# Kernel tuning notes

Hardware: AMD Instinct MI355X
Metric: run time of the kernel (lower is better)

Reference implementation:

```python
import jax, jax.numpy as jnp
import numpy as np

D = 512       # input_embedding_dimensions
H = 2         # num_heads
HD = D // H   # head_dim = 256
B = 16
S = 1194      # max_sequence_length


def setup_inputs() -> dict:
    key = jax.random.key(0)
    k1, k2, k3, k4, k5 = jax.random.split(key, 5)
    scale_in = 1.0 / np.sqrt(D)
    return {
        "positional_embeddings": jax.random.normal(k1, (B, S, D), dtype=jnp.float32),
        "W_qkv": jax.random.uniform(k2, (D, 3 * D), minval=-scale_in, maxval=scale_in, dtype=jnp.float32),
        "b_qkv": jax.random.uniform(k3, (3 * D,), minval=-scale_in, maxval=scale_in, dtype=jnp.float32),
        "W_out": jax.random.uniform(k4, (D, D), minval=-scale_in, maxval=scale_in, dtype=jnp.float32),
        "b_out": jax.random.uniform(k5, (D,), minval=-scale_in, maxval=scale_in, dtype=jnp.float32),
    }


def reference(positional_embeddings, W_qkv, b_qkv, W_out, b_out):
    x = positional_embeddings              # [B, S, D]
    b, s, _ = x.shape
    qkv = x @ W_qkv + b_qkv                # [B, S, 3D]
    q, k, v = jnp.split(qkv, 3, axis=-1)

    def split_heads(t):
        return t.reshape(b, s, H, HD).transpose(0, 2, 1, 3)  # [B, H, S, HD]

    q, k, v = split_heads(q), split_heads(k), split_heads(v)
    scores = jnp.einsum("bhqd,bhkd->bhqk", q, k) / jnp.sqrt(jnp.float32(HD))
    causal = jnp.tril(jnp.ones((s, s), dtype=bool))          # [S, S]
    scores = jnp.where(causal[None, None, :, :], scores, -jnp.inf)
    att = jax.nn.softmax(scores, axis=-1)                    # [B, H, S, S]
    out = jnp.einsum("bhqk,bhkd->bhqd", att, v)              # [B, H, S, HD]
    out = out.transpose(0, 2, 1, 3).reshape(b, s, D)         # [B, S, D]
    return out @ W_out + b_out
```

## Files before the change

kernel.cpp:

```cpp
#include <hip/hip_runtime.h>
#include <stdint.h>

#define D_    512
#define H_    2
#define HD_   256
#define B_    16
#define S_    1194
#define MTOK  19104
#define MPAD  19200
#define SPAD  1216
#define NQKV  1536
#define NKT   38
#define LOG2E 1.44269504088896340736f

typedef unsigned short u16;
typedef __attribute__((ext_vector_type(8))) short bf16x8;
typedef __attribute__((ext_vector_type(4))) float f32x4;

__device__ inline u16 f2bf(float x) {
  union { float f; unsigned u; } c; c.f = x;
  unsigned r = c.u + 0x7fffu + ((c.u >> 16) & 1u);
  return (u16)(r >> 16);
}

__device__ inline void async_copy16(void* lds, const void* g) {
  __builtin_amdgcn_global_load_lds(
      (__attribute__((address_space(1))) void*)(g),
      (__attribute__((address_space(3))) void*)(lds),
      16, 0, 0);
}

__global__ void convert_kernel(const float* __restrict__ X,
                               const float* __restrict__ Wqkv,
                               const float* __restrict__ Wout,
                               u16* __restrict__ Xf,
                               u16* __restrict__ Wqf,
                               u16* __restrict__ Wof) {
  const int NXG = MPAD * 64;
  const int NQG = 12 * 8 * 16 * 64;
  const int NOG = 4 * 8 * 16 * 64;
  const int TOT = NXG + NQG + NOG;
  int stride = gridDim.x * blockDim.x;
  for (int g = blockIdx.x * blockDim.x + threadIdx.x; g < TOT; g += stride) {
    if (g < NXG) {
      int lane = g & 63, f = (g >> 6) & 15, kt = (g >> 10) & 7, mt = g >> 13;
      int i = mt * 128 + (f & 7) * 16 + (lane & 15);
      int k = kt * 64 + (f >> 3) * 32 + (lane >> 4) * 8;
      bf16x8 o;
      if (i < MTOK) {
        f32x4 v0 = *(const f32x4*)&X[(size_t)i * 512 + k];
        f32x4 v1 = *(const f32x4*)&X[(size_t)i * 512 + k + 4];
#pragma unroll
        for (int e = 0; e < 4; ++e) { o[e] = (short)f2bf(v0[e]); o[4 + e] = (short)f2bf(v1[e]); }
      } else {
#pragma unroll
        for (int e = 0; e < 8; ++e) o[e] = 0;
      }
      *(bf16x8*)&Xf[(size_t)g * 8] = o;
    } else if (g < NXG + NQG) {
      int gg = g - NXG;
      int lane = gg & 63, f = (gg >> 6) & 15, kt = (gg >> 10) & 7, nt = gg >> 13;
      int j = nt * 128 + (f & 7) * 16 + (lane & 15);
      int k = kt * 64 + (f >> 3) * 32 + (lane >> 4) * 8;
      bf16x8 o;
#pragma unroll
      for (int e = 0; e < 8; ++e) o[e] = (short)f2bf(Wqkv[(size_t)(k + e) * NQKV + j]);
      *(bf16x8*)&Wqf[(size_t)gg * 8] = o;
    } else {
      int gg = g - NXG - NQG;
      int lane = gg & 63, f = (gg >> 6) & 15, kt = (gg >> 10) & 7, nt = gg >> 13;
      int j = nt * 128 + (f & 7) * 16 + (lane & 15);
      int k = kt * 64 + (f >> 3) * 32 + (lane >> 4) * 8;
      bf16x8 o;
#pragma unroll
      for (int e = 0; e < 8; ++e) o[e] = (short)f2bf(Wout[(size_t)(k + e) * 512 + j]);
      *(bf16x8*)&Wof[(size_t)gg * 8] = o;
    }
  }
}

template<int MODE>
__global__ __launch_bounds__(256, 2) void gemm_kernel(
    const u16* __restrict__ Af, const u16* __restrict__ Bf,
    const float* __restrict__ bias, int nb,
    u16* __restrict__ Qb, u16* __restrict__ Kf, u16* __restrict__ Vf,
    float* __restrict__ Cout)
{
  __shared__ u16 ldsA[16 * 512];
  __shared__ u16 ldsB[16 * 512];

  const int t  = threadIdx.x;
  const int l  = t & 63;
  const int w  = t >> 6;
  const int lr = l >> 4, lc = l & 15;

  const int nwg = gridDim.x;
  const int qq = nwg >> 3, rr8 = nwg & 7;
  const int xcd = blockIdx.x & 7, off = blockIdx.x >> 3;
  const int wgid = (xcd < rr8 ? xcd * (qq + 1) : rr8 * (qq + 1) + (xcd - rr8) * qq) + off;
  const int m0 = (wgid / nb) * 128;
  const int n0 = (wgid % nb) * 128;

  const u16* pA = Af + ((size_t)(m0 >> 7) * 128 + w) * 512 + l * 8;
  const u16* pB = Bf + ((size_t)(n0 >> 7) * 128 + w) * 512 + l * 8;

  f32x4 acc[4][4] = {};

  for (int kt = 0; kt < 8; ++kt) {
    __syncthreads();
    const u16* qA = pA + kt * 8192;
    const u16* qB = pB + kt * 8192;
#pragma unroll
    for (int c = 0; c < 4; ++c) {
      async_copy16(&ldsA[(c * 4 + w) * 512], qA + c * 2048);
      async_copy16(&ldsB[(c * 4 + w) * 512], qB + c * 2048);
    }
    __syncthreads();
#pragma unroll
    for (int kk = 0; kk < 2; ++kk) {
      bf16x8 af[4], bfr[4];
#pragma unroll
      for (int m = 0; m < 4; ++m)
        af[m] = *(bf16x8*)&ldsA[((kk * 8 + (w >> 1) * 4 + m) * 64 + l) * 8];
#pragma unroll
      for (int n = 0; n < 4; ++n)
        bfr[n] = *(bf16x8*)&ldsB[((kk * 8 + (w & 1) * 4 + n) * 64 + l) * 8];
      __builtin_amdgcn_s_setprio(1);
#pragma unroll
      for (int m = 0; m < 4; ++m)
#pragma unroll
        for (int n = 0; n < 4; ++n)
          acc[m][n] = __builtin_amdgcn_mfma_f32_16x16x32_bf16(af[m], bfr[n], acc[m][n], 0, 0, 0);
      __builtin_amdgcn_s_setprio(0);
    }
  }

  int jv[4]; float bj[4];
#pragma unroll
  for (int n = 0; n < 4; ++n) { jv[n] = n0 + (w & 1) * 64 + n * 16 + lc; bj[n] = bias[jv[n]]; }

#pragma unroll
  for (int m = 0; m < 4; ++m) {
#pragma unroll
    for (int r = 0; r < 4; ++r) {
      int i = m0 + (w >> 1) * 64 + m * 16 + lr * 4 + r;
      if (i >= MTOK) continue;
      if (MODE == 0) {
        int b = i / S_, s = i - b * S_;
        int stK  = s >> 5;
        int nfs  = (s >> 4) & 1;
        int lisK = s & 15;
        int lvhi = (s >> 3) & 3;
        int es   = s & 7;
#pragma unroll
        for (int n = 0; n < 4; ++n) {
          int j = jv[n];
          int which = j >> 9, h = (j >> 8) & 1, d = j & 255;
          int bh = b * H_ + h;
          u16 v = f2bf(acc[m][n][r] + bj[n]);
          if (which == 0) {
            Qb[((size_t)(bh * SPAD + s)) * HD_ + d] = v;
          } else if (which == 1) {
            Kf[(((size_t)(bh * NKT + stK)) * 16 + (d >> 5) * 2 + nfs) * 512 +
               (((d >> 3) & 3) * 16 + lisK) * 8 + (d & 7)] = v;
          } else {
            Vf[(((size_t)(bh * NKT + stK)) * 16 + (d >> 4)) * 512 +
               (lvhi * 16 + (d & 15)) * 8 + es] = v;
          }
        }
      } else {
#pragma unroll
        for (int n = 0; n < 4; ++n)
          Cout[(size_t)i * D_ + jv[n]] = acc[m][n][r] + bj[n];
      }
    }
  }
}

__global__ __launch_bounds__(256, 2) void attn_kernel(
    const u16* __restrict__ Qb, const u16* __restrict__ Kf,
    const u16* __restrict__ Vf, u16* __restrict__ Obf)
{
  __shared__ u16 ldsK[2][16 * 512];
  __shared__ u16 ldsP[4][16 * 36];

  const int id   = blockIdx.x;
  const int xcd  = id & 7;
  const int slot = id >> 3;
  const int bh   = xcd + 8 * (slot / 19);
  const int qt   = 18 - (slot % 19);
  const int q0   = qt * 64;
  const int nkv  = 2 * qt + 2;
  const int t  = threadIdx.x, l = t & 63, w = t >> 6;
  const int lr = l >> 4, lc = l & 15;
  const int wq0 = q0 + w * 16;
  const int qrow_l = wq0 + lc;

  bf16x8 qf[8];
  const u16* qbase = Qb + (size_t)(bh * SPAD + qrow_l) * HD_ + lr * 8;
#pragma unroll
  for (int kb = 0; kb < 8; ++kb)
    qf[kb] = *(const bf16x8*)(qbase + kb * 32);

  f32x4 oacc[16] = {};
  float mrow = -1e30f, lsum = 0.f;

  {
    const u16* kb_ = Kf + (((size_t)(bh * NKT)) * 16 + w) * 512 + l * 8;
#pragma unroll
    for (int c = 0; c < 4; ++c)
      async_copy16(&ldsK[0][(c * 4 + w) * 512], kb_ + c * 2048);
  }
  __syncthreads();

  for (int kt = 0; kt < nkv; ++kt) {
    const int cur = kt & 1;

    bf16x8 vfr[16];
    {
      const u16* vb_ = Vf + (((size_t)(bh * NKT + kt)) * 16) * 512 + l * 8;
#pragma unroll
      for (int nf = 0; nf < 16; ++nf)
        vfr[nf] = *(const bf16x8*)(vb_ + nf * 512);
    }

    if (kt + 1 < nkv) {
      const u16* kb_ = Kf + (((size_t)(bh * NKT + kt + 1)) * 16 + w) * 512 + l * 8;
#pragma unroll
      for (int c = 0; c < 4; ++c)
        async_copy16(&ldsK[cur ^ 1][(c * 4 + w) * 512], kb_ + c * 2048);
    }

    f32x4 sacc[2] = {};
    __builtin_amdgcn_s_setprio(1);
#pragma unroll
    for (int kb = 0; kb < 8; ++kb) {
#pragma unroll
      for (int nf = 0; nf < 2; ++nf) {
        bf16x8 kf = *(bf16x8*)&ldsK[cur][((kb * 2 + nf) * 64 + l) * 8];
        sacc[nf] = __builtin_amdgcn_mfma_f32_16x16x32_bf16(kf, qf[kb], sacc[nf], 0, 0, 0);
      }
    }
    __builtin_amdgcn_s_setprio(0);

    const int kv0 = kt * 32;
    float sv[2][4];
    float pm = -1e30f;
    if (kv0 + 31 <= wq0) {
#pragma unroll
      for (int nf = 0; nf < 2; ++nf)
#pragma unroll
        for (int r = 0; r < 4; ++r) {
          float v = sacc[nf][r] * 0.0625f;
          sv[nf][r] = v;
          pm = fmaxf(pm, v);
        }
    } else {
#pragma unroll
      for (int nf = 0; nf < 2; ++nf)
#pragma unroll
        for (int r = 0; r < 4; ++r) {
          int kv = kv0 + nf * 16 + lr * 4 + r;
          float v = ((kv <= qrow_l) && (kv < S_)) ? sacc[nf][r] * 0.0625f : -1e30f;
          sv[nf][r] = v;
          pm = fmaxf(pm, v);
        }
    }
    pm = fmaxf(pm, __shfl_xor(pm, 16));
    pm = fmaxf(pm, __shfl_xor(pm, 32));

    bool skip = (pm <= mrow + 8.0f);
    if (!__all(skip)) {
      float mn = fmaxf(mrow, pm);
      float sc = exp2f((mrow - mn) * LOG2E);
      mrow = mn;
      lsum *= sc;
#pragma unroll
      for (int nf = 0; nf < 16; ++nf)
#pragma unroll
        for (int r = 0; r < 4; ++r) oacc[nf][r] *= sc;
    }

#pragma unroll
    for (int nf = 0; nf < 2; ++nf) {
      float p0 = exp2f((sv[nf][0] - mrow) * LOG2E);
      float p1 = exp2f((sv[nf][1] - mrow) * LOG2E);
      float p2 = exp2f((sv[nf][2] - mrow) * LOG2E);
      float p3 = exp2f((sv[nf][3] - mrow) * LOG2E);
      lsum += (p0 + p1) + (p2 + p3);
      uint64_t pk = (uint64_t)f2bf(p0) | ((uint64_t)f2bf(p1) << 16) |
                    ((uint64_t)f2bf(p2) << 32) | ((uint64_t)f2bf(p3) << 48);
      *(uint64_t*)&ldsP[w][lc * 36 + nf * 16 + lr * 4] = pk;
    }

    __syncthreads();

    bf16x8 pf = *(bf16x8*)&ldsP[w][lc * 36 + lr * 8];
    __builtin_amdgcn_s_setprio(1);
#pragma unroll
    for (int nf = 0; nf < 16; ++nf)
      oacc[nf] = __builtin_amdgcn_mfma_f32_16x16x32_bf16(vfr[nf], pf, oacc[nf], 0, 0, 0);
    __builtin_amdgcn_s_setprio(0);
  }

  float s = lsum;
  s += __shfl_xor(s, 16);
  s += __shfl_xor(s, 32);
  float inv = 1.0f / s;

  const int b = bh >> 1, h = bh & 1;
  if (qrow_l < S_) {
    int i = b * S_ + qrow_l;
    int it = i >> 7, mf = (i >> 4) & 7, li = i & 15;
#pragma unroll
    for (int nf = 0; nf < 16; ++nf) {
#pragma unroll
      for (int r = 0; r < 4; ++r) {
        int j = h * HD_ + nf * 16 + lr * 4 + r;
        size_t addr = (((size_t)(it * 8 + (j >> 6))) * 16 + ((j >> 5) & 1) * 8 + mf) * 512 +
                      (((j >> 3) & 3) * 16 + li) * 8 + (j & 7);
        Obf[addr] = f2bf(oacc[nf][r] * inv);
      }
    }
  }
}

extern "C" void kernel_launch(void* const* d_in, const int* in_sizes, int n_in,
                              void* d_out, int out_size, void* d_ws, size_t ws_size,
                              hipStream_t stream) {
  const float* X    = (const float*)d_in[0];
  const float* Wqkv = (const float*)d_in[1];
  const float* bqkv = (const float*)d_in[2];
  const float* Wout = (const float*)d_in[3];
  const float* bout = (const float*)d_in[4];
  float* out = (float*)d_out;

  char* ws = (char*)d_ws;
  u16* Xf  = (u16*)ws;  ws += (size_t)MPAD * D_ * 2;
  u16* Wqf = (u16*)ws;  ws += (size_t)NQKV * D_ * 2;
  u16* Wof = (u16*)ws;  ws += (size_t)D_ * D_ * 2;
  u16* Qb  = (u16*)ws;  ws += (size_t)B_ * H_ * SPAD * HD_ * 2;
  u16* Kf  = (u16*)ws;  ws += (size_t)B_ * H_ * SPAD * HD_ * 2;
  u16* Vf  = (u16*)ws;  ws += (size_t)B_ * H_ * SPAD * HD_ * 2;
  u16* Obf = (u16*)ws;  ws += (size_t)MPAD * D_ * 2;

  convert_kernel<<<2048, 256, 0, stream>>>(X, Wqkv, Wout, Xf, Wqf, Wof);
  gemm_kernel<0><<<1800, 256, 0, stream>>>(Xf, Wqf, bqkv, 12, Qb, Kf, Vf, nullptr);
  attn_kernel<<<608, 256, 0, stream>>>(Qb, Kf, Vf, Obf);
  gemm_kernel<1><<<600, 256, 0, stream>>>(Obf, Wof, bout, 4, nullptr, nullptr, nullptr, out);
}
```

Measured before the change: 153.0 us.

## Load K fragments directly into registers and drop LDS double-buffering and block barrier

The attention kernel no longer stages K tiles in shared memory through async double-buffered copies. Each wave loads its K fragments from global memory straight into registers, reusing the same register array for V after the QK MFMAs. This lowers register pressure and removes the per-iteration __syncthreads, since the P buffer is per-wave. In exchange, every wave now redundantly reads the full K tile from global/L2, and the overlap between K prefetch and compute is lost.

```diff
diff --git a/kernel.cpp b/kernel.cpp
--- a/kernel.cpp
+++ b/kernel.cpp
@@ -181,7 +181,6 @@
     const u16* __restrict__ Qb, const u16* __restrict__ Kf,
     const u16* __restrict__ Vf, u16* __restrict__ Obf)
 {
-  __shared__ u16 ldsK[2][16 * 512];
   __shared__ u16 ldsP[4][16 * 36];
 
   const int id   = blockIdx.x;
@@ -205,30 +204,16 @@
   f32x4 oacc[16] = {};
   float mrow = -1e30f, lsum = 0.f;
 
-  {
-    const u16* kb_ = Kf + (((size_t)(bh * NKT)) * 16 + w) * 512 + l * 8;
-#pragma unroll
-    for (int c = 0; c < 4; ++c)
-      async_copy16(&ldsK[0][(c * 4 + w) * 512], kb_ + c * 2048);
-  }
-  __syncthreads();
+  const u16* kroot = Kf + (((size_t)(bh * NKT)) * 16) * 512 + l * 8;
+  const u16* vroot = Vf + (((size_t)(bh * NKT)) * 16) * 512 + l * 8;
 
   for (int kt = 0; kt < nkv; ++kt) {
-    const int cur = kt & 1;
-
-    bf16x8 vfr[16];
+    bf16x8 kv[16];
     {
-      const u16* vb_ = Vf + (((size_t)(bh * NKT + kt)) * 16) * 512 + l * 8;
-#pragma unroll
-      for (int nf = 0; nf < 16; ++nf)
-        vfr[nf] = *(const bf16x8*)(vb_ + nf * 512);
-    }
-
-    if (kt + 1 < nkv) {
-      const u16* kb_ = Kf + (((size_t)(bh * NKT + kt + 1)) * 16 + w) * 512 + l * 8;
-#pragma unroll
-      for (int c = 0; c < 4; ++c)
-        async_copy16(&ldsK[cur ^ 1][(c * 4 + w) * 512], kb_ + c * 2048);
+      const u16* kb_ = kroot + (size_t)kt * 16 * 512;
+#pragma unroll
+      for (int f = 0; f < 16; ++f)
+        kv[f] = *(const bf16x8*)(kb_ + f * 512);
     }
 
     f32x4 sacc[2] = {};
@@ -236,12 +221,17 @@
 #pragma unroll
     for (int kb = 0; kb < 8; ++kb) {
 #pragma unroll
-      for (int nf = 0; nf < 2; ++nf) {
-        bf16x8 kf = *(bf16x8*)&ldsK[cur][((kb * 2 + nf) * 64 + l) * 8];
-        sacc[nf] = __builtin_amdgcn_mfma_f32_16x16x32_bf16(kf, qf[kb], sacc[nf], 0, 0, 0);
-      }
+      for (int nf = 0; nf < 2; ++nf)
+        sacc[nf] = __builtin_amdgcn_mfma_f32_16x16x32_bf16(kv[kb * 2 + nf], qf[kb], sacc[nf], 0, 0, 0);
     }
     __builtin_amdgcn_s_setprio(0);
+
+    {
+      const u16* vb_ = vroot + (size_t)kt * 16 * 512;
+#pragma unroll
+      for (int f = 0; f < 16; ++f)
+        kv[f] = *(const bf16x8*)(vb_ + f * 512);
+    }
 
     const int kv0 = kt * 32;
     float sv[2][4];
@@ -260,8 +250,8 @@
       for (int nf = 0; nf < 2; ++nf)
 #pragma unroll
         for (int r = 0; r < 4; ++r) {
-          int kv = kv0 + nf * 16 + lr * 4 + r;
-          float v = ((kv <= qrow_l) && (kv < S_)) ? sacc[nf][r] * 0.0625f : -1e30f;
+          int kvi = kv0 + nf * 16 + lr * 4 + r;
+          float v = ((kvi <= qrow_l) && (kvi < S_)) ? sacc[nf][r] * 0.0625f : -1e30f;
           sv[nf][r] = v;
           pm = fmaxf(pm, v);
         }
@@ -293,13 +283,11 @@
       *(uint64_t*)&ldsP[w][lc * 36 + nf * 16 + lr * 4] = pk;
     }
 
-    __syncthreads();
-
     bf16x8 pf = *(bf16x8*)&ldsP[w][lc * 36 + lr * 8];
     __builtin_amdgcn_s_setprio(1);
 #pragma unroll
     for (int nf = 0; nf < 16; ++nf)
-      oacc[nf] = __builtin_amdgcn_mfma_f32_16x16x32_bf16(vfr[nf], pf, oacc[nf], 0, 0, 0);
+      oacc[nf] = __builtin_amdgcn_mfma_f32_16x16x32_bf16(kv[nf], pf, oacc[nf], 0, 0, 0);
     __builtin_amdgcn_s_setprio(0);
   }
 
```

After: 159.8 us. 1.04x slower.

## Split attention KV loop across two wave groups and vectorize GEMM epilogue stores

Applied to the files above, without the earlier changes.

The attention kernel now runs 512 threads per block. Two groups of four waves each take alternating 32-key tiles, and their partial softmax states are merged through LDS at the end. V fragments for the next tile are prefetched into registers after the PV MFMAs. The QKV/out GEMMs swap MFMA operands for the non-V bands, so each lane holds four consecutive columns and can write packed 64-bit or float4 stores instead of scalar 16-bit ones; the V band writes packed 32-bit pairs. The aim is more parallelism per query tile in attention and fewer, wider global stores in the epilogues, at the cost of extra LDS use, a merge step, and higher register pressure.

```diff
diff --git a/kernel.cpp b/kernel.cpp
--- a/kernel.cpp
+++ b/kernel.cpp
@@ -14,6 +14,7 @@
 #define LOG2E 1.44269504088896340736f
 
 typedef unsigned short u16;
+typedef unsigned int u32;
 typedef __attribute__((ext_vector_type(8))) short bf16x8;
 typedef __attribute__((ext_vector_type(4))) float f32x4;
 
@@ -100,6 +101,7 @@
   const int wgid = (xcd < rr8 ? xcd * (qq + 1) : rr8 * (qq + 1) + (xcd - rr8) * qq) + off;
   const int m0 = (wgid / nb) * 128;
   const int n0 = (wgid % nb) * 128;
+  const bool vband = (MODE == 0) && ((wgid % nb) >= 8);
 
   const u16* pA = Af + ((size_t)(m0 >> 7) * 128 + w) * 512 + l * 8;
   const u16* pB = Bf + ((size_t)(n0 >> 7) * 128 + w) * 512 + l * 8;
@@ -126,63 +128,97 @@
       for (int n = 0; n < 4; ++n)
         bfr[n] = *(bf16x8*)&ldsB[((kk * 8 + (w & 1) * 4 + n) * 64 + l) * 8];
       __builtin_amdgcn_s_setprio(1);
-#pragma unroll
-      for (int m = 0; m < 4; ++m)
-#pragma unroll
-        for (int n = 0; n < 4; ++n)
-          acc[m][n] = __builtin_amdgcn_mfma_f32_16x16x32_bf16(af[m], bfr[n], acc[m][n], 0, 0, 0);
+      if (!vband) {
+#pragma unroll
+        for (int m = 0; m < 4; ++m)
+#pragma unroll
+          for (int n = 0; n < 4; ++n)
+            acc[m][n] = __builtin_amdgcn_mfma_f32_16x16x32_bf16(bfr[n], af[m], acc[m][n], 0, 0, 0);
+      } else {
+#pragma unroll
+        for (int m = 0; m < 4; ++m)
+#pragma unroll
+          for (int n = 0; n < 4; ++n)
+            acc[m][n] = __builtin_amdgcn_mfma_f32_16x16x32_bf16(af[m], bfr[n], acc[m][n], 0, 0, 0);
+      }
       __builtin_amdgcn_s_setprio(0);
     }
   }
 
-  int jv[4]; float bj[4];
-#pragma unroll
-  for (int n = 0; n < 4; ++n) { jv[n] = n0 + (w & 1) * 64 + n * 16 + lc; bj[n] = bias[jv[n]]; }
-
-#pragma unroll
-  for (int m = 0; m < 4; ++m) {
-#pragma unroll
-    for (int r = 0; r < 4; ++r) {
-      int i = m0 + (w >> 1) * 64 + m * 16 + lr * 4 + r;
+  if (MODE == 1) {
+#pragma unroll
+    for (int m = 0; m < 4; ++m) {
+      int i = m0 + (w >> 1) * 64 + m * 16 + lc;
       if (i >= MTOK) continue;
-      if (MODE == 0) {
-        int b = i / S_, s = i - b * S_;
-        int stK  = s >> 5;
-        int nfs  = (s >> 4) & 1;
-        int lisK = s & 15;
-        int lvhi = (s >> 3) & 3;
-        int es   = s & 7;
+#pragma unroll
+      for (int n = 0; n < 4; ++n) {
+        int jb = n0 + (w & 1) * 64 + n * 16 + lr * 4;
+        f32x4 bv = *(const f32x4*)&bias[jb];
+        f32x4 o;
+#pragma unroll
+        for (int r = 0; r < 4; ++r) o[r] = acc[m][n][r] + bv[r];
+        *(f32x4*)&Cout[(size_t)i * D_ + jb] = o;
+      }
+    }
+  } else if (!vband) {
+#pragma unroll
+    for (int m = 0; m < 4; ++m) {
+      int i = m0 + (w >> 1) * 64 + m * 16 + lc;
+      if (i >= MTOK) continue;
+      int b = i / S_, s = i - b * S_;
+      int stK = s >> 5, nfs = (s >> 4) & 1, lisK = s & 15;
+#pragma unroll
+      for (int n = 0; n < 4; ++n) {
+        int jb = n0 + (w & 1) * 64 + n * 16 + lr * 4;
+        f32x4 bv = *(const f32x4*)&bias[jb];
+        uint64_t pk = 0;
+#pragma unroll
+        for (int r = 0; r < 4; ++r)
+          pk |= (uint64_t)f2bf(acc[m][n][r] + bv[r]) << (16 * r);
+        int which = jb >> 9, h = (jb >> 8) & 1, d = jb & 255;
+        int bh = b * H_ + h;
+        if (which == 0) {
+          *(uint64_t*)&Qb[(size_t)(bh * SPAD + s) * HD_ + d] = pk;
+        } else {
+          *(uint64_t*)&Kf[(((size_t)(bh * NKT + stK)) * 16 + (d >> 5) * 2 + nfs) * 512 +
+                          (((d >> 3) & 3) * 16 + lisK) * 8 + (d & 7)] = pk;
+        }
+      }
+    }
+  } else {
+    int jv[4]; float bj[4];
+#pragma unroll
+    for (int n = 0; n < 4; ++n) { jv[n] = n0 + (w & 1) * 64 + n * 16 + lc; bj[n] = bias[jv[n]]; }
+#pragma unroll
+    for (int m = 0; m < 4; ++m) {
+#pragma unroll
+      for (int rp = 0; rp < 4; rp += 2) {
+        int i0 = m0 + (w >> 1) * 64 + m * 16 + lr * 4 + rp;
+        if (i0 >= MTOK) continue;
+        int b = i0 / S_, s = i0 - b * S_;
+        int stK = s >> 5, lvhi = (s >> 3) & 3, es = s & 7;
 #pragma unroll
         for (int n = 0; n < 4; ++n) {
           int j = jv[n];
-          int which = j >> 9, h = (j >> 8) & 1, d = j & 255;
+          int h = (j >> 8) & 1, d = j & 255;
           int bh = b * H_ + h;
-          u16 v = f2bf(acc[m][n][r] + bj[n]);
-          if (which == 0) {
-            Qb[((size_t)(bh * SPAD + s)) * HD_ + d] = v;
-          } else if (which == 1) {
-            Kf[(((size_t)(bh * NKT + stK)) * 16 + (d >> 5) * 2 + nfs) * 512 +
-               (((d >> 3) & 3) * 16 + lisK) * 8 + (d & 7)] = v;
-          } else {
-            Vf[(((size_t)(bh * NKT + stK)) * 16 + (d >> 4)) * 512 +
-               (lvhi * 16 + (d & 15)) * 8 + es] = v;
-          }
+          u32 pk = (u32)f2bf(acc[m][n][rp] + bj[n]) |
+                   ((u32)f2bf(acc[m][n][rp + 1] + bj[n]) << 16);
+          *(u32*)&Vf[(((size_t)(bh * NKT + stK)) * 16 + (d >> 4)) * 512 +
+                     (lvhi * 16 + (d & 15)) * 8 + es] = pk;
         }
-      } else {
-#pragma unroll
-        for (int n = 0; n < 4; ++n)
-          Cout[(size_t)i * D_ + jv[n]] = acc[m][n][r] + bj[n];
-      }
-    }
-  }
-}
-
-__global__ __launch_bounds__(256, 2) void attn_kernel(
+      }
+    }
+  }
+}
+
+__global__ __launch_bounds__(512, 2) void attn_kernel(
     const u16* __restrict__ Qb, const u16* __restrict__ Kf,
     const u16* __restrict__ Vf, u16* __restrict__ Obf)
 {
-  __shared__ u16 ldsK[2][16 * 512];
-  __shared__ u16 ldsP[4][16 * 36];
+  __shared__ u16 ldsK[2][32 * 512];
+  __shared__ u16 ldsP[8][16 * 36];
+  __shared__ float ldsML[8][128];
 
   const int id   = blockIdx.x;
   const int xcd  = id & 7;
@@ -191,9 +227,11 @@
   const int qt   = 18 - (slot % 19);
   const int q0   = qt * 64;
   const int nkv  = 2 * qt + 2;
+  const int ns   = nkv >> 1;
   const int t  = threadIdx.x, l = t & 63, w = t >> 6;
+  const int qg = w & 3, par = w >> 2;
   const int lr = l >> 4, lc = l & 15;
-  const int wq0 = q0 + w * 16;
+  const int wq0 = q0 + qg * 16;
   const int qrow_l = wq0 + lc;
 
   bf16x8 qf[8];
@@ -205,30 +243,33 @@
   f32x4 oacc[16] = {};
   float mrow = -1e30f, lsum = 0.f;
 
+  const u16* kroot = Kf + (size_t)(bh * NKT) * 8192 + l * 8;
+  const u16* vroot = Vf + (size_t)(bh * NKT) * 8192 + l * 8;
+
+#pragma unroll
+  for (int c = 0; c < 4; ++c) {
+    int g = w * 4 + c;
+    async_copy16(&ldsK[0][g * 512], kroot + (g >> 4) * 8192 + (g & 15) * 512);
+  }
+  bf16x8 vfr[16];
   {
-    const u16* kb_ = Kf + (((size_t)(bh * NKT)) * 16 + w) * 512 + l * 8;
-#pragma unroll
-    for (int c = 0; c < 4; ++c)
-      async_copy16(&ldsK[0][(c * 4 + w) * 512], kb_ + c * 2048);
+    const u16* vb_ = vroot + (size_t)par * 8192;
+#pragma unroll
+    for (int f = 0; f < 16; ++f) vfr[f] = *(const bf16x8*)(vb_ + f * 512);
   }
   __syncthreads();
 
-  for (int kt = 0; kt < nkv; ++kt) {
-    const int cur = kt & 1;
-
-    bf16x8 vfr[16];
-    {
-      const u16* vb_ = Vf + (((size_t)(bh * NKT + kt)) * 16) * 512 + l * 8;
-#pragma unroll
-      for (int nf = 0; nf < 16; ++nf)
-        vfr[nf] = *(const bf16x8*)(vb_ + nf * 512);
-    }
-
-    if (kt + 1 < nkv) {
-      const u16* kb_ = Kf + (((size_t)(bh * NKT + kt + 1)) * 16 + w) * 512 + l * 8;
-#pragma unroll
-      for (int c = 0; c < 4; ++c)
-        async_copy16(&ldsK[cur ^ 1][(c * 4 + w) * 512], kb_ + c * 2048);
+  for (int s = 0; s < ns; ++s) {
+    const int cur = s & 1;
+
+    if (s + 1 < ns) {
+      const int T = 2 * s + 2;
+#pragma unroll
+      for (int c = 0; c < 4; ++c) {
+        int g = w * 4 + c;
+        async_copy16(&ldsK[cur ^ 1][g * 512],
+                     kroot + (size_t)(T + (g >> 4)) * 8192 + (g & 15) * 512);
+      }
     }
 
     f32x4 sacc[2] = {};
@@ -237,13 +278,13 @@
     for (int kb = 0; kb < 8; ++kb) {
 #pragma unroll
       for (int nf = 0; nf < 2; ++nf) {
-        bf16x8 kf = *(bf16x8*)&ldsK[cur][((kb * 2 + nf) * 64 + l) * 8];
+        bf16x8 kf = *(bf16x8*)&ldsK[cur][((par * 16 + kb * 2 + nf) * 64 + l) * 8];
         sacc[nf] = __builtin_amdgcn_mfma_f32_16x16x32_bf16(kf, qf[kb], sacc[nf], 0, 0, 0);
       }
     }
     __builtin_amdgcn_s_setprio(0);
 
-    const int kv0 = kt * 32;
+    const int kv0 = (2 * s + par) * 32;
     float sv[2][4];
     float pm = -1e30f;
     if (kv0 + 31 <= wq0) {
@@ -260,8 +301,8 @@
       for (int nf = 0; nf < 2; ++nf)
 #pragma unroll
         for (int r = 0; r < 4; ++r) {
-          int kv = kv0 + nf * 16 + lr * 4 + r;
-          float v = ((kv <= qrow_l) && (kv < S_)) ? sacc[nf][r] * 0.0625f : -1e30f;
+          int kvi = kv0 + nf * 16 + lr * 4 + r;
+          float v = ((kvi <= qrow_l) && (kvi < S_)) ? sacc[nf][r] * 0.0625f : -1e30f;
           sv[nf][r] = v;
           pm = fmaxf(pm, v);
         }
@@ -301,25 +342,54 @@
     for (int nf = 0; nf < 16; ++nf)
       oacc[nf] = __builtin_amdgcn_mfma_f32_16x16x32_bf16(vfr[nf], pf, oacc[nf], 0, 0, 0);
     __builtin_amdgcn_s_setprio(0);
-  }
-
-  float s = lsum;
-  s += __shfl_xor(s, 16);
-  s += __shfl_xor(s, 32);
-  float inv = 1.0f / s;
-
-  const int b = bh >> 1, h = bh & 1;
-  if (qrow_l < S_) {
-    int i = b * S_ + qrow_l;
-    int it = i >> 7, mf = (i >> 4) & 7, li = i & 15;
-#pragma unroll
-    for (int nf = 0; nf < 16; ++nf) {
-#pragma unroll
-      for (int r = 0; r < 4; ++r) {
-        int j = h * HD_ + nf * 16 + lr * 4 + r;
-        size_t addr = (((size_t)(it * 8 + (j >> 6))) * 16 + ((j >> 5) & 1) * 8 + mf) * 512 +
-                      (((j >> 3) & 3) * 16 + li) * 8 + (j & 7);
-        Obf[addr] = f2bf(oacc[nf][r] * inv);
+
+    if (s + 1 < ns) {
+      const u16* vb_ = vroot + (size_t)(2 * (s + 1) + par) * 8192;
+#pragma unroll
+      for (int f = 0; f < 16; ++f) vfr[f] = *(const bf16x8*)(vb_ + f * 512);
+    }
+  }
+
+  lsum += __shfl_xor(lsum, 16);
+  lsum += __shfl_xor(lsum, 32);
+  __syncthreads();
+
+  float* ldsC = (float*)&ldsK[0][0];
+  if (par == 1) {
+#pragma unroll
+    for (int nf = 0; nf < 16; ++nf)
+      *(f32x4*)&ldsC[((size_t)(qg * 64 + l)) * 64 + nf * 4] = oacc[nf];
+    ldsML[w][l * 2]     = mrow;
+    ldsML[w][l * 2 + 1] = lsum;
+  }
+  __syncthreads();
+
+  if (par == 0) {
+    float m2 = ldsML[w + 4][l * 2];
+    float l2 = ldsML[w + 4][l * 2 + 1];
+    float m  = fmaxf(mrow, m2);
+    float a1 = exp2f((mrow - m) * LOG2E);
+    float a2 = exp2f((m2 - m) * LOG2E);
+    float lt = a1 * lsum + a2 * l2;
+    float inv = 1.0f / lt;
+
+    const int b = bh >> 1, h = bh & 1;
+    if (qrow_l < S_) {
+      int i = b * S_ + qrow_l;
+      int it = i >> 7, mf = (i >> 4) & 7, li = i & 15;
+#pragma unroll
+      for (int nf = 0; nf < 16; ++nf) {
+        f32x4 o2 = *(f32x4*)&ldsC[((size_t)(qg * 64 + l)) * 64 + nf * 4];
+        int j0 = h * HD_ + nf * 16 + lr * 4;
+        uint64_t pk = 0;
+#pragma unroll
+        for (int r = 0; r < 4; ++r) {
+          float val = (a1 * oacc[nf][r] + a2 * o2[r]) * inv;
+          pk |= (uint64_t)f2bf(val) << (16 * r);
+        }
+        size_t addr = (((size_t)(it * 8 + (j0 >> 6))) * 16 + ((j0 >> 5) & 1) * 8 + mf) * 512 +
+                      (((j0 >> 3) & 3) * 16 + li) * 8 + (j0 & 7);
+        *(uint64_t*)&Obf[addr] = pk;
       }
     }
   }
@@ -346,6 +416,6 @@
 
   convert_kernel<<<2048, 256, 0, stream>>>(X, Wqkv, Wout, Xf, Wqf, Wof);
   gemm_kernel<0><<<1800, 256, 0, stream>>>(Xf, Wqf, bqkv, 12, Qb, Kf, Vf, nullptr);
-  attn_kernel<<<608, 256, 0, stream>>>(Qb, Kf, Vf, Obf);
+  attn_kernel<<<608, 512, 0, stream>>>(Qb, Kf, Vf, Obf);
   gemm_kernel<1><<<600, 256, 0, stream>>>(Obf, Wof, bout, 4, nullptr, nullptr, nullptr, out);
 }
```

Result: slower. 169.8 us (+11.0%).
